# Kernel tuning notes

Hardware: AMD Instinct MI355X
Metric: run time of the kernel (lower is better)

Reference implementation:

```python
import jax, jax.numpy as jnp
import numpy as np

N_USERS, N_ITEMS = 6000, 4000
EPS = 1e-8


def _cosine_similarity(X):
    # rows of X normalized to unit length, then dense gram matrix [n, n]
    norms = jnp.linalg.norm(X, axis=1, keepdims=True) + EPS
    Xn = X / norms
    return Xn @ Xn.T


def _top_k_adjacency(S, k):
    # faithful, vectorized version of the per-row Python loop in the torch code:
    # take top-(k+1), drop the self index, keep the first k remaining entries,
    # scatter values into a sparse-pattern adjacency, then symmetrize.
    n = S.shape[0]
    k_actual = min(k + 1, n)
    vals, idx = jax.lax.top_k(S, k_actual)          # [n, k+1]
    rows = jnp.arange(n)[:, None]                    # [n, 1]
    valid = idx != rows                              # exclude self
    # keep only the first k valid entries per row ( [:k] truncation in torch )
    keep = valid & (jnp.cumsum(valid, axis=1) <= k)
    vals = jnp.where(keep, vals, 0.0)
    adj = jnp.zeros_like(S).at[rows, idx].set(vals)  # indices distinct per row
    return (adj + adj.T) * 0.5


def _sym_normalize(A):
    row_sums = A.sum(axis=1, keepdims=True) + EPS
    col_sums = A.sum(axis=0, keepdims=True) + EPS
    return A / jnp.sqrt(row_sums) / jnp.sqrt(col_sums)


def setup_inputs() -> dict:
    key = jax.random.key(0)
    R = jax.random.uniform(key, (N_USERS, N_ITEMS), dtype=jnp.float32)
    return {"R": R, "k_users": 50, "k_items": 20}


def reference(R, k_users, k_items):
    # user-user graph from cosine similarity over interaction rows
    user_adj = _sym_normalize(_top_k_adjacency(_cosine_similarity(R), k_users))
    # item-item graph from cosine similarity over interaction columns
    item_adj = _sym_normalize(_top_k_adjacency(_cosine_similarity(R.T), k_items))
    # two-sided spectral-style propagation of the interaction signal
    out = user_adj @ (R @ item_adj)                  # [n_users, n_items]
    return out
```

## Files before the change

kernel.cpp:

```cpp
#include <hip/hip_runtime.h>
#include <math.h>

#define EPS 1e-8f

constexpr int N_USERS = 6000;
constexpr int N_ITEMS = 4000;
constexpr int NU_P = 6016;
constexpr int NI_P = 4096;

typedef __bf16 bf16_8 __attribute__((ext_vector_type(8)));
typedef float f32_4 __attribute__((ext_vector_type(4)));
typedef int i32x4 __attribute__((ext_vector_type(4)));

__device__ __forceinline__ void stage16(const void* g, void* l) {
  __builtin_amdgcn_global_load_lds(
      (const __attribute__((address_space(1))) void*)g,
      (__attribute__((address_space(3))) void*)l, 16, 0, 0);
}

__device__ __forceinline__ int xcd_swz(int p, int nwg) {
  return (p & 7) * (nwg >> 3) + (p >> 3);
}

__device__ __forceinline__ void tri_decode(int p, int& by, int& bx) {
  int r = (int)((sqrtf(8.f * p + 1.f) - 1.f) * 0.5f);
  while ((r + 1) * (r + 2) / 2 <= p) r++;
  while (r * (r + 1) / 2 > p) r--;
  by = r;
  bx = p - r * (r + 1) / 2;
}

__device__ __forceinline__ void grp_decode(int p, int nby, int nbx, int& by,
                                           int& bx) {
  const int G = 8;
  const int wide = G * nbx;
  const int band = p / wide;
  const int rem = p - band * wide;
  const int h = min(G, nby - band * G);
  by = band * G + rem % h;
  bx = rem / h;
}

template <int KK, int LDA, int LDB, int LDC, int OUTBF16>
__global__ __launch_bounds__(256) void mfma_prop_bf16(
    const __bf16* __restrict__ A, const __bf16* __restrict__ B,
    float* __restrict__ Cf, __bf16* __restrict__ Cb, int M, int N, int nby,
    int nbx) {
  __shared__ __bf16 sA[2][128 * 32];
  __shared__ __bf16 sB[2][128 * 32];

  int by, bx;
  grp_decode(xcd_swz(blockIdx.x, gridDim.x), nby, nbx, by, bx);

  const int tid = threadIdx.x;
  const int lane = tid & 63;
  const int wave = tid >> 6;
  const int wm = (wave >> 1) * 64;
  const int wn = (wave & 1) * 64;
  const int lm = lane & 15;
  const int kg = lane >> 4;
  const long row0 = (long)by * 128;
  const long col0 = (long)bx * 128;

  f32_4 acc[4][4];
#pragma unroll
  for (int i = 0; i < 4; i++)
#pragma unroll
    for (int j = 0; j < 4; j++) acc[i][j] = (f32_4){0.f, 0.f, 0.f, 0.f};

  const int c0 = tid, c1 = tid + 256;
  const int r0c = c0 >> 2, j0c = ((c0 & 3) - (r0c >> 1)) & 3;
  const int r1c = c1 >> 2, j1c = ((c1 & 3) - (r1c >> 1)) & 3;

  int offA[4], offB[4];
#pragma unroll
  for (int i = 0; i < 4; i++) {
    const int ra = wm + i * 16 + lm;
    const int rb = wn + i * 16 + lm;
    offA[i] = (ra * 4 + ((kg + (ra >> 1)) & 3)) * 8;
    offB[i] = (rb * 4 + ((kg + (rb >> 1)) & 3)) * 8;
  }

  const __bf16* a0 = A + (row0 + r0c) * LDA + j0c * 8;
  const __bf16* a1 = A + (row0 + r1c) * LDA + j1c * 8;
  const __bf16* b0 = B + (col0 + r0c) * LDB + j0c * 8;
  const __bf16* b1 = B + (col0 + r1c) * LDB + j1c * 8;

  for (int k0 = 0; k0 < KK; k0 += 64) {
    stage16(a0 + k0, &sA[0][c0 * 8]);
    stage16(a1 + k0, &sA[0][c1 * 8]);
    stage16(b0 + k0, &sB[0][c0 * 8]);
    stage16(b1 + k0, &sB[0][c1 * 8]);
    stage16(a0 + k0 + 32, &sA[1][c0 * 8]);
    stage16(a1 + k0 + 32, &sA[1][c1 * 8]);
    stage16(b0 + k0 + 32, &sB[1][c0 * 8]);
    stage16(b1 + k0 + 32, &sB[1][c1 * 8]);
    __syncthreads();

#pragma unroll
    for (int h = 0; h < 2; h++) {
      bf16_8 a[4], b[4];
#pragma unroll
      for (int i = 0; i < 4; i++) {
        a[i] = *(const bf16_8*)&sA[h][offA[i]];
        b[i] = *(const bf16_8*)&sB[h][offB[i]];
      }
#pragma unroll
      for (int i = 0; i < 4; i++)
#pragma unroll
        for (int j = 0; j < 4; j++)
          acc[i][j] = __builtin_amdgcn_mfma_f32_16x16x32_bf16(a[i], b[j],
                                                              acc[i][j], 0, 0,
                                                              0);
    }
    __syncthreads();
  }

#pragma unroll
  for (int i = 0; i < 4; i++)
#pragma unroll
    for (int j = 0; j < 4; j++)
#pragma unroll
      for (int r = 0; r < 4; r++) {
        const long gm = row0 + wm + i * 16 + kg * 4 + r;
        const long gn = col0 + wn + j * 16 + lm;
        if (gm < M && gn < N) {
          if (OUTBF16)
            Cb[gm * LDC + gn] = (__bf16)acc[i][j][r];
          else
            Cf[gm * LDC + gn] = acc[i][j][r];
        }
      }
}

template <int KK, int LD, int LDC>
__global__ __launch_bounds__(256) void mfma_gram_i8(
    const signed char* __restrict__ Q, const float* __restrict__ sv,
    float* __restrict__ C, int Nn, float negq) {
  __shared__ signed char sA[2][128 * 64];
  __shared__ signed char sB[2][128 * 64];

  int by, bx;
  tri_decode(xcd_swz(blockIdx.x, gridDim.x), by, bx);

  const int tid = threadIdx.x;
  const int lane = tid & 63;
  const int wave = tid >> 6;
  const int wm = (wave >> 1) * 64;
  const int wn = (wave & 1) * 64;
  const int lm = lane & 15;
  const int kg = lane >> 4;
  const long row0 = (long)by * 128;
  const long col0 = (long)bx * 128;
  const float scale = 1.f / (254.f * 254.f);

  i32x4 acc[4][4];
#pragma unroll
  for (int i = 0; i < 4; i++)
#pragma unroll
    for (int j = 0; j < 4; j++) acc[i][j] = (i32x4){0, 0, 0, 0};

  const int c0 = tid, c1 = tid + 256;
  const int r0c = c0 >> 2, j0c = ((c0 & 3) - (r0c >> 1)) & 3;
  const int r1c = c1 >> 2, j1c = ((c1 & 3) - (r1c >> 1)) & 3;

  int offA[4], offB[4];
#pragma unroll
  for (int i = 0; i < 4; i++) {
    const int ra = wm + i * 16 + lm;
    const int rb = wn + i * 16 + lm;
    offA[i] = (ra * 4 + ((kg + (ra >> 1)) & 3)) * 16;
    offB[i] = (rb * 4 + ((kg + (rb >> 1)) & 3)) * 16;
  }

  const signed char* a0 = Q + (row0 + r0c) * LD + j0c * 16;
  const signed char* a1 = Q + (row0 + r1c) * LD + j1c * 16;
  const signed char* b0 = Q + (col0 + r0c) * LD + j0c * 16;
  const signed char* b1 = Q + (col0 + r1c) * LD + j1c * 16;

  for (int k0 = 0; k0 < KK; k0 += 128) {
    stage16(a0 + k0, &sA[0][c0 * 16]);
    stage16(a1 + k0, &sA[0][c1 * 16]);
    stage16(b0 + k0, &sB[0][c0 * 16]);
    stage16(b1 + k0, &sB[0][c1 * 16]);
    stage16(a0 + k0 + 64, &sA[1][c0 * 16]);
    stage16(a1 + k0 + 64, &sA[1][c1 * 16]);
    stage16(b0 + k0 + 64, &sB[1][c0 * 16]);
    stage16(b1 + k0 + 64, &sB[1][c1 * 16]);
    __syncthreads();

#pragma unroll
    for (int h = 0; h < 2; h++) {
      i32x4 a[4], b[4];
#pragma unroll
      for (int i = 0; i < 4; i++) {
        a[i] = *(const i32x4*)&sA[h][offA[i]];
        b[i] = *(const i32x4*)&sB[h][offB[i]];
      }
#pragma unroll
      for (int i = 0; i < 4; i++)
#pragma unroll
        for (int j = 0; j < 4; j++)
          acc[i][j] = __builtin_amdgcn_mfma_i32_16x16x64_i8(a[i], b[j],
                                                            acc[i][j], 0, 0, 0);
    }
    __syncthreads();
  }

#pragma unroll
  for (int i = 0; i < 4; i++)
#pragma unroll
    for (int j = 0; j < 4; j++)
#pragma unroll
      for (int r = 0; r < 4; r++) {
        const long gm = row0 + wm + i * 16 + kg * 4 + r;
        const long gn = col0 + wn + j * 16 + lm;
        if (gm < Nn && gn < Nn)
          C[gm * LDC + gn] = fmaf((float)acc[i][j][r], scale,
                                  0.5f * (sv[gm] + sv[gn]) + negq);
      }
}

__global__ __launch_bounds__(256) void pad_quant_kernel(
    const float* __restrict__ R, __bf16* __restrict__ H,
    signed char* __restrict__ Qp, int M, int N, int Np) {
  const int r = blockIdx.y;
  const int c = blockIdx.x * 256 + threadIdx.x;
  if (c >= Np) return;
  const bool in = (r < M && c < N);
  const float v = in ? R[(long)r * N + c] : 0.f;
  H[(long)r * Np + c] = (__bf16)v;
  Qp[(long)r * Np + c] =
      in ? (signed char)__float2int_rn((v - 0.5f) * 254.f) : (signed char)0;
}

__global__ __launch_bounds__(256) void transpose_quant_kernel(
    const float* __restrict__ R, signed char* __restrict__ Qp, int M, int N,
    int Mp, int Np) {
  __shared__ float tile[32][33];
  const int tx = threadIdx.x & 31;
  const int ty = threadIdx.x >> 5;
  const int ri = blockIdx.y * 32;
  const int ci = blockIdx.x * 32;
#pragma unroll
  for (int k = 0; k < 4; k++) {
    const int r = ri + ty + k * 8, c = ci + tx;
    tile[ty + k * 8][tx] = (r < M && c < N) ? R[(long)r * N + c] : 0.f;
  }
  __syncthreads();
#pragma unroll
  for (int k = 0; k < 4; k++) {
    const int orow = ci + ty + k * 8;
    const int ocol = ri + tx;
    if (orow < Np && ocol < Mp) {
      const bool in = (orow < N && ocol < M);
      const float v = tile[tx][ty + k * 8];
      Qp[(long)orow * Mp + ocol] =
          in ? (signed char)__float2int_rn((v - 0.5f) * 254.f) : (signed char)0;
    }
  }
}

__global__ __launch_bounds__(256) void mirror_kernel(float* __restrict__ S,
                                                     int n) {
  __shared__ float tile[32][33];
  int by, bx;
  tri_decode(blockIdx.x, by, bx);
  const int tj = by + 1, ti = bx;
  const int sr = tj * 32, sc = ti * 32;
  const int tx = threadIdx.x & 31;
  const int ty = threadIdx.x >> 5;
#pragma unroll
  for (int k = 0; k < 4; k++) {
    const int r = sr + ty + k * 8, c = sc + tx;
    tile[ty + k * 8][tx] = (r < n && c < n) ? S[(long)r * n + c] : 0.f;
  }
  __syncthreads();
#pragma unroll
  for (int k = 0; k < 4; k++) {
    const int r = sc + ty + k * 8, c = sr + tx;
    if (r < n && c < n) S[(long)r * n + c] = tile[tx][ty + k * 8];
  }
}

__global__ __launch_bounds__(256) void row_norm_sum(
    const float* __restrict__ R, float* __restrict__ inv_n,
    float* __restrict__ sv, int M, int K) {
  __shared__ float redA[256];
  __shared__ float redB[256];
  const int row = blockIdx.x;
  float s2 = 0.f, s1 = 0.f;
  for (int j = threadIdx.x; j < K; j += 256) {
    const float v = R[(long)row * K + j];
    s2 = fmaf(v, v, s2);
    s1 += v;
  }
  redA[threadIdx.x] = s2;
  redB[threadIdx.x] = s1;
  __syncthreads();
  for (int o = 128; o > 0; o >>= 1) {
    if (threadIdx.x < o) {
      redA[threadIdx.x] += redA[threadIdx.x + o];
      redB[threadIdx.x] += redB[threadIdx.x + o];
    }
    __syncthreads();
  }
  if (threadIdx.x == 0) {
    inv_n[row] = 1.f / (sqrtf(redA[0]) + EPS);
    sv[row] = redB[0];
  }
}

__global__ __launch_bounds__(256) void col_sums_kernel(
    const float* __restrict__ R, float* __restrict__ acc2,
    float* __restrict__ acc1, int M, int N, int rows_per_chunk) {
  const int j = blockIdx.x * 256 + threadIdx.x;
  if (j >= N) return;
  const int r0 = blockIdx.y * rows_per_chunk;
  const int r1 = min(M, r0 + rows_per_chunk);
  float s2 = 0.f, s1 = 0.f;
  for (int i = r0; i < r1; i++) {
    const float v = R[(long)i * N + j];
    s2 = fmaf(v, v, s2);
    s1 += v;
  }
  atomicAdd(&acc2[j], s2);
  atomicAdd(&acc1[j], s1);
}

__global__ __launch_bounds__(256) void inv_norm_finalize(
    const float* __restrict__ acc, float* __restrict__ inv_n, int n) {
  const int i = blockIdx.x * 256 + threadIdx.x;
  if (i < n) inv_n[i] = 1.f / (sqrtf(acc[i]) + EPS);
}

__global__ __launch_bounds__(64) void topk_kernel(
    float* __restrict__ G, const float* __restrict__ inv_n,
    __bf16* __restrict__ adj, float* __restrict__ rowsum,
    float* __restrict__ colsum, int n, int np, const int* __restrict__ kptr) {
  const int row = blockIdx.x;
  const int lane = threadIdx.x;
  const int k = *kptr;
  const float invr = inv_n[row];

  float v0 = -INFINITY, v1 = -INFINITY, v2 = -INFINITY, v3 = -INFINITY;
  int i0 = n, i1 = n, i2 = n, i3 = n;

  for (int j = lane; j < n; j += 64) {
    const float v =
        (j == row) ? -INFINITY : G[(long)row * n + j] * invr * inv_n[j];
    if (v > v3) {
      if (v > v1) {
        if (v > v0) {
          v3 = v2; i3 = i2; v2 = v1; i2 = i1; v1 = v0; i1 = i0; v0 = v; i0 = j;
        } else {
          v3 = v2; i3 = i2; v2 = v1; i2 = i1; v1 = v; i1 = j;
        }
      } else {
        if (v > v2) {
          v3 = v2; i3 = i2; v2 = v; i2 = j;
        } else {
          v3 = v; i3 = j;
        }
      }
    }
  }

  float rsum = 0.f;
  for (int t = 0; t < k; t++) {
    float v = v0;
    int i = i0;
#pragma unroll
    for (int off = 32; off > 0; off >>= 1) {
      const float ov = __shfl_xor(v, off);
      const int oi = __shfl_xor(i, off);
      if (ov > v || (ov == v && oi < i)) { v = ov; i = oi; }
    }
    if (lane == 0) {
      adj[(long)row * np + i] = (__bf16)v;
      atomicAdd(&colsum[i], v);
      rsum += v;
    }
    if ((i & 63) == lane) {
      G[(long)row * n + i] = -INFINITY;
      v0 = v1; i0 = i1; v1 = v2; i1 = i2; v2 = v3; i2 = i3;
      v3 = -INFINITY; i3 = n;
      if (i0 == n) {
        for (int j = lane; j < n; j += 64) {
          const float vv =
              (j == row) ? -INFINITY : G[(long)row * n + j] * invr * inv_n[j];
          if (vv > v3) {
            if (vv > v1) {
              if (vv > v0) {
                v3 = v2; i3 = i2; v2 = v1; i2 = i1; v1 = v0; i1 = i0;
                v0 = vv; i0 = j;
              } else {
                v3 = v2; i3 = i2; v2 = v1; i2 = i1; v1 = vv; i1 = j;
              }
            } else {
              if (vv > v2) {
                v3 = v2; i3 = i2; v2 = vv; i2 = j;
              } else {
                v3 = vv; i3 = j;
              }
            }
          }
        }
      }
    }
  }
  if (lane == 0) rowsum[row] = rsum;
}

__global__ __launch_bounds__(256) void finalize_kernel(
    const float* __restrict__ rs, const float* __restrict__ cs,
    float* __restrict__ f, int n) {
  const int i = blockIdx.x * 256 + threadIdx.x;
  if (i < n) f[i] = rsqrtf(0.5f * (rs[i] + cs[i]) + EPS);
}

__global__ __launch_bounds__(256) void symscale_kernel(
    __bf16* __restrict__ adj, const float* __restrict__ f, int n, int np) {
  const long idx = (long)blockIdx.x * 256 + threadIdx.x;
  if (idx >= (long)np * np) return;
  const int i = (int)(idx / np);
  const int j = (int)(idx % np);
  if (j <= i || i >= n || j >= n) return;
  const float a = (float)adj[(long)i * np + j];
  const float b = (float)adj[(long)j * np + i];
  const float m = 0.5f * (a + b) * f[i] * f[j];
  adj[(long)i * np + j] = (__bf16)m;
  adj[(long)j * np + i] = (__bf16)m;
}

extern "C" void kernel_launch(void* const* d_in, const int* in_sizes, int n_in,
                              void* d_out, int out_size, void* d_ws,
                              size_t ws_size, hipStream_t stream) {
  const float* R = (const float*)d_in[0];
  const int* k_users_p = (const int*)d_in[1];
  const int* k_items_p = (const int*)d_in[2];
  float* out = (float*)d_out;
  const int NU = N_USERS, NI = N_ITEMS;

  char* ws = (char*)d_ws;
  float* invNu = (float*)(ws + 0);
  float* invNi = (float*)(ws + 32768);
  float* rsU = (float*)(ws + 65536);
  float* csU = (float*)(ws + 98304);
  float* rsI = (float*)(ws + 131072);
  float* csI = (float*)(ws + 163840);
  float* fU = (float*)(ws + 196608);
  float* fI = (float*)(ws + 229376);
  float* nrmI = (float*)(ws + 262144);
  float* svU = (float*)(ws + 294912);
  float* svI = (float*)(ws + 327680);
  const long MB = 1000000L;
  __bf16* Rh = (__bf16*)(ws + 1 * MB);
  signed char* Uh = (signed char*)(ws + 51 * MB);
  float* Su = (float*)(ws + 77 * MB);
  signed char* IhT = (signed char*)(ws + 103 * MB);
  float* Si = (float*)(ws + 128 * MB);
  __bf16* adjIb = (__bf16*)(ws + 222 * MB);
  __bf16* adjUb = (__bf16*)(ws + 256 * MB);
  __bf16* Tt = (__bf16*)(ws + 77 * MB);

  row_norm_sum<<<NU, 256, 0, stream>>>(R, invNu, svU, NU, NI);
  hipMemsetAsync(nrmI, 0, NI * sizeof(float), stream);
  hipMemsetAsync(svI, 0, NI * sizeof(float), stream);
  col_sums_kernel<<<dim3((NI + 255) / 256, 60), 256, 0, stream>>>(R, nrmI, svI,
                                                                  NU, NI, 100);
  inv_norm_finalize<<<(NI + 255) / 256, 256, 0, stream>>>(nrmI, invNi, NI);
  pad_quant_kernel<<<dim3(NI_P / 256, NU_P), 256, 0, stream>>>(R, Rh, Uh, NU,
                                                               NI, NI_P);
  transpose_quant_kernel<<<dim3(NI_P / 32, NU_P / 32), 256, 0, stream>>>(
      R, IhT, NU, NI, NU_P, NI_P);

  mfma_gram_i8<NU_P, NU_P, N_ITEMS><<<32 * 33 / 2, 256, 0, stream>>>(
      IhT, svI, Si, NI, -0.25f * (float)NU);
  {
    const int T = (NI + 31) / 32;
    mirror_kernel<<<T * (T - 1) / 2, 256, 0, stream>>>(Si, NI);
  }
  hipMemsetAsync(adjIb, 0, (long)NI_P * NI_P * sizeof(__bf16), stream);
  hipMemsetAsync(csI, 0, NI * sizeof(float), stream);
  topk_kernel<<<NI, 64, 0, stream>>>(Si, invNi, adjIb, rsI, csI, NI, NI_P,
                                     k_items_p);
  finalize_kernel<<<(NI + 255) / 256, 256, 0, stream>>>(rsI, csI, fI, NI);
  {
    const long tot = (long)NI_P * NI_P;
    symscale_kernel<<<(tot + 255) / 256, 256, 0, stream>>>(adjIb, fI, NI, NI_P);
  }

  mfma_gram_i8<NI_P, NI_P, N_USERS><<<47 * 48 / 2, 256, 0, stream>>>(
      Uh, svU, Su, NU, -0.25f * (float)NI);
  {
    const int T = (NU + 31) / 32;
    mirror_kernel<<<T * (T - 1) / 2, 256, 0, stream>>>(Su, NU);
  }
  hipMemsetAsync(adjUb, 0, (long)NU_P * NU_P * sizeof(__bf16), stream);
  hipMemsetAsync(csU, 0, NU * sizeof(float), stream);
  topk_kernel<<<NU, 64, 0, stream>>>(Su, invNu, adjUb, rsU, csU, NU, NU_P,
                                     k_users_p);
  finalize_kernel<<<(NU + 255) / 256, 256, 0, stream>>>(rsU, csU, fU, NU);
  {
    const long tot = (long)NU_P * NU_P;
    symscale_kernel<<<(tot + 255) / 256, 256, 0, stream>>>(adjUb, fU, NU, NU_P);
  }

  mfma_prop_bf16<NI_P, NI_P, NI_P, NU_P, 1><<<32 * 47, 256, 0, stream>>>(
      adjIb, Rh, nullptr, Tt, NI_P, NU_P, 32, 47);
  mfma_prop_bf16<NU_P, NU_P, NU_P, N_ITEMS, 0><<<47 * 32, 256, 0, stream>>>(
      adjUb, Tt, out, nullptr, NU, NI, 47, 32);
}
```

Measured before the change: 1.780 ms.

## Double-buffer LDS staging to overlap global loads with MFMA compute

Both GEMM kernels change from loading two K-halves and then computing them behind a barrier to a ping-pong pipeline. The next K-slice is staged asynchronously into the alternate LDS buffer while the current slice is computed, with one barrier per step. The goal is to hide global-to-LDS latency behind MFMA work. In exchange there are twice as many loop iterations and barriers per unit of K, and each iteration stages less data.

```diff
diff --git a/kernel.cpp b/kernel.cpp
--- a/kernel.cpp
+++ b/kernel.cpp
@@ -86,35 +86,37 @@
   const __bf16* b0 = B + (col0 + r0c) * LDB + j0c * 8;
   const __bf16* b1 = B + (col0 + r1c) * LDB + j1c * 8;
 
-  for (int k0 = 0; k0 < KK; k0 += 64) {
-    stage16(a0 + k0, &sA[0][c0 * 8]);
-    stage16(a1 + k0, &sA[0][c1 * 8]);
-    stage16(b0 + k0, &sB[0][c0 * 8]);
-    stage16(b1 + k0, &sB[0][c1 * 8]);
-    stage16(a0 + k0 + 32, &sA[1][c0 * 8]);
-    stage16(a1 + k0 + 32, &sA[1][c1 * 8]);
-    stage16(b0 + k0 + 32, &sB[1][c0 * 8]);
-    stage16(b1 + k0 + 32, &sB[1][c1 * 8]);
+  auto stage_phase = [&](int buf, int k0) {
+    stage16(a0 + k0, &sA[buf][c0 * 8]);
+    stage16(a1 + k0, &sA[buf][c1 * 8]);
+    stage16(b0 + k0, &sB[buf][c0 * 8]);
+    stage16(b1 + k0, &sB[buf][c1 * 8]);
+  };
+  auto compute_phase = [&](int buf) {
+    bf16_8 a[4], b[4];
+#pragma unroll
+    for (int i = 0; i < 4; i++) {
+      a[i] = *(const bf16_8*)&sA[buf][offA[i]];
+      b[i] = *(const bf16_8*)&sB[buf][offB[i]];
+    }
+#pragma unroll
+    for (int i = 0; i < 4; i++)
+#pragma unroll
+      for (int j = 0; j < 4; j++)
+        acc[i][j] = __builtin_amdgcn_mfma_f32_16x16x32_bf16(a[i], b[j],
+                                                            acc[i][j], 0, 0, 0);
+  };
+
+  stage_phase(0, 0);
+  __syncthreads();
+  int cur = 0;
+  for (int k0 = 32; k0 < KK; k0 += 32) {
+    stage_phase(cur ^ 1, k0);
+    compute_phase(cur);
     __syncthreads();
-
-#pragma unroll
-    for (int h = 0; h < 2; h++) {
-      bf16_8 a[4], b[4];
-#pragma unroll
-      for (int i = 0; i < 4; i++) {
-        a[i] = *(const bf16_8*)&sA[h][offA[i]];
-        b[i] = *(const bf16_8*)&sB[h][offB[i]];
-      }
-#pragma unroll
-      for (int i = 0; i < 4; i++)
-#pragma unroll
-        for (int j = 0; j < 4; j++)
-          acc[i][j] = __builtin_amdgcn_mfma_f32_16x16x32_bf16(a[i], b[j],
-                                                              acc[i][j], 0, 0,
-                                                              0);
-    }
-    __syncthreads();
-  }
+    cur ^= 1;
+  }
+  compute_phase(cur);
 
 #pragma unroll
   for (int i = 0; i < 4; i++)
@@ -178,34 +180,37 @@
   const signed char* b0 = Q + (col0 + r0c) * LD + j0c * 16;
   const signed char* b1 = Q + (col0 + r1c) * LD + j1c * 16;
 
-  for (int k0 = 0; k0 < KK; k0 += 128) {
-    stage16(a0 + k0, &sA[0][c0 * 16]);
-    stage16(a1 + k0, &sA[0][c1 * 16]);
-    stage16(b0 + k0, &sB[0][c0 * 16]);
-    stage16(b1 + k0, &sB[0][c1 * 16]);
-    stage16(a0 + k0 + 64, &sA[1][c0 * 16]);
-    stage16(a1 + k0 + 64, &sA[1][c1 * 16]);
-    stage16(b0 + k0 + 64, &sB[1][c0 * 16]);
-    stage16(b1 + k0 + 64, &sB[1][c1 * 16]);
+  auto stage_phase = [&](int buf, int k0) {
+    stage16(a0 + k0, &sA[buf][c0 * 16]);
+    stage16(a1 + k0, &sA[buf][c1 * 16]);
+    stage16(b0 + k0, &sB[buf][c0 * 16]);
+    stage16(b1 + k0, &sB[buf][c1 * 16]);
+  };
+  auto compute_phase = [&](int buf) {
+    i32x4 a[4], b[4];
+#pragma unroll
+    for (int i = 0; i < 4; i++) {
+      a[i] = *(const i32x4*)&sA[buf][offA[i]];
+      b[i] = *(const i32x4*)&sB[buf][offB[i]];
+    }
+#pragma unroll
+    for (int i = 0; i < 4; i++)
+#pragma unroll
+      for (int j = 0; j < 4; j++)
+        acc[i][j] = __builtin_amdgcn_mfma_i32_16x16x64_i8(a[i], b[j],
+                                                          acc[i][j], 0, 0, 0);
+  };
+
+  stage_phase(0, 0);
+  __syncthreads();
+  int cur = 0;
+  for (int k0 = 64; k0 < KK; k0 += 64) {
+    stage_phase(cur ^ 1, k0);
+    compute_phase(cur);
     __syncthreads();
-
-#pragma unroll
-    for (int h = 0; h < 2; h++) {
-      i32x4 a[4], b[4];
-#pragma unroll
-      for (int i = 0; i < 4; i++) {
-        a[i] = *(const i32x4*)&sA[h][offA[i]];
-        b[i] = *(const i32x4*)&sB[h][offB[i]];
-      }
-#pragma unroll
-      for (int i = 0; i < 4; i++)
-#pragma unroll
-        for (int j = 0; j < 4; j++)
-          acc[i][j] = __builtin_amdgcn_mfma_i32_16x16x64_i8(a[i], b[j],
-                                                            acc[i][j], 0, 0, 0);
-    }
-    __syncthreads();
-  }
+    cur ^= 1;
+  }
+  compute_phase(cur);
 
 #pragma unroll
   for (int i = 0; i < 4; i++)
```

Result: no change. 1.787 ms (+0.4%).

## Double-buffer LDS staging in bf16 and int8 GEMM mainloops

Applied to the files above, without the earlier changes.

Both GEMM kernels used to load two K-halves into LDS, wait at a barrier, then compute, so global-to-LDS loads never overlapped the MFMA work. The loops are now software-pipelined with two LDS buffers: the next chunk is staged into one buffer while the other is consumed, with a prologue and epilogue. This aims to hide global load latency behind matrix math. The risk is a race: the compute on the current buffer is not separated by a barrier from the async global_load_lds writes into the other buffer, and the fill issued just before each compute runs with no vmcnt wait before the following barrier.

```diff
diff --git a/kernel.cpp b/kernel.cpp
--- a/kernel.cpp
+++ b/kernel.cpp
@@ -86,35 +86,44 @@
   const __bf16* b0 = B + (col0 + r0c) * LDB + j0c * 8;
   const __bf16* b1 = B + (col0 + r1c) * LDB + j1c * 8;
 
-  for (int k0 = 0; k0 < KK; k0 += 64) {
-    stage16(a0 + k0, &sA[0][c0 * 8]);
-    stage16(a1 + k0, &sA[0][c1 * 8]);
-    stage16(b0 + k0, &sB[0][c0 * 8]);
-    stage16(b1 + k0, &sB[0][c1 * 8]);
-    stage16(a0 + k0 + 32, &sA[1][c0 * 8]);
-    stage16(a1 + k0 + 32, &sA[1][c1 * 8]);
-    stage16(b0 + k0 + 32, &sB[1][c0 * 8]);
-    stage16(b1 + k0 + 32, &sB[1][c1 * 8]);
+#define PROP_STAGE(BUF, K0)                  \
+  do {                                       \
+    stage16(a0 + (K0), &sA[BUF][c0 * 8]);    \
+    stage16(a1 + (K0), &sA[BUF][c1 * 8]);    \
+    stage16(b0 + (K0), &sB[BUF][c0 * 8]);    \
+    stage16(b1 + (K0), &sB[BUF][c1 * 8]);    \
+  } while (0)
+
+#define PROP_COMPUTE(BUF)                                                   \
+  do {                                                                      \
+    bf16_8 a[4], b[4];                                                      \
+    _Pragma("unroll") for (int i = 0; i < 4; i++) {                         \
+      a[i] = *(const bf16_8*)&sA[BUF][offA[i]];                             \
+      b[i] = *(const bf16_8*)&sB[BUF][offB[i]];                             \
+    }                                                                       \
+    _Pragma("unroll") for (int i = 0; i < 4; i++) _Pragma("unroll") for (   \
+        int j = 0; j < 4; j++) acc[i][j] =                                  \
+        __builtin_amdgcn_mfma_f32_16x16x32_bf16(a[i], b[j], acc[i][j], 0,   \
+                                                0, 0);                      \
+  } while (0)
+
+  PROP_STAGE(0, 0);
+  __syncthreads();
+  for (int k0 = 32; k0 < KK - 32; k0 += 64) {
+    PROP_STAGE(1, k0);
+    PROP_COMPUTE(0);
     __syncthreads();
-
-#pragma unroll
-    for (int h = 0; h < 2; h++) {
-      bf16_8 a[4], b[4];
-#pragma unroll
-      for (int i = 0; i < 4; i++) {
-        a[i] = *(const bf16_8*)&sA[h][offA[i]];
-        b[i] = *(const bf16_8*)&sB[h][offB[i]];
-      }
-#pragma unroll
-      for (int i = 0; i < 4; i++)
-#pragma unroll
-        for (int j = 0; j < 4; j++)
-          acc[i][j] = __builtin_amdgcn_mfma_f32_16x16x32_bf16(a[i], b[j],
-                                                              acc[i][j], 0, 0,
-                                                              0);
-    }
+    PROP_STAGE(0, k0 + 32);
+    PROP_COMPUTE(1);
     __syncthreads();
   }
+  PROP_STAGE(1, KK - 32);
+  PROP_COMPUTE(0);
+  __syncthreads();
+  PROP_COMPUTE(1);
+
+#undef PROP_STAGE
+#undef PROP_COMPUTE
 
 #pragma unroll
   for (int i = 0; i < 4; i++)
@@ -178,34 +187,44 @@
   const signed char* b0 = Q + (col0 + r0c) * LD + j0c * 16;
   const signed char* b1 = Q + (col0 + r1c) * LD + j1c * 16;
 
-  for (int k0 = 0; k0 < KK; k0 += 128) {
-    stage16(a0 + k0, &sA[0][c0 * 16]);
-    stage16(a1 + k0, &sA[0][c1 * 16]);
-    stage16(b0 + k0, &sB[0][c0 * 16]);
-    stage16(b1 + k0, &sB[0][c1 * 16]);
-    stage16(a0 + k0 + 64, &sA[1][c0 * 16]);
-    stage16(a1 + k0 + 64, &sA[1][c1 * 16]);
-    stage16(b0 + k0 + 64, &sB[1][c0 * 16]);
-    stage16(b1 + k0 + 64, &sB[1][c1 * 16]);
+#define GRAM_STAGE(BUF, K0)                   \
+  do {                                        \
+    stage16(a0 + (K0), &sA[BUF][c0 * 16]);    \
+    stage16(a1 + (K0), &sA[BUF][c1 * 16]);    \
+    stage16(b0 + (K0), &sB[BUF][c0 * 16]);    \
+    stage16(b1 + (K0), &sB[BUF][c1 * 16]);    \
+  } while (0)
+
+#define GRAM_COMPUTE(BUF)                                                 \
+  do {                                                                    \
+    i32x4 a[4], b[4];                                                     \
+    _Pragma("unroll") for (int i = 0; i < 4; i++) {                       \
+      a[i] = *(const i32x4*)&sA[BUF][offA[i]];                            \
+      b[i] = *(const i32x4*)&sB[BUF][offB[i]];                            \
+    }                                                                     \
+    _Pragma("unroll") for (int i = 0; i < 4; i++) _Pragma("unroll") for ( \
+        int j = 0; j < 4; j++) acc[i][j] =                                \
+        __builtin_amdgcn_mfma_i32_16x16x64_i8(a[i], b[j], acc[i][j], 0,   \
+                                              0, 0);                      \
+  } while (0)
+
+  GRAM_STAGE(0, 0);
+  __syncthreads();
+  for (int k0 = 64; k0 < KK - 64; k0 += 128) {
+    GRAM_STAGE(1, k0);
+    GRAM_COMPUTE(0);
     __syncthreads();
-
-#pragma unroll
-    for (int h = 0; h < 2; h++) {
-      i32x4 a[4], b[4];
-#pragma unroll
-      for (int i = 0; i < 4; i++) {
-        a[i] = *(const i32x4*)&sA[h][offA[i]];
-        b[i] = *(const i32x4*)&sB[h][offB[i]];
-      }
-#pragma unroll
-      for (int i = 0; i < 4; i++)
-#pragma unroll
-        for (int j = 0; j < 4; j++)
-          acc[i][j] = __builtin_amdgcn_mfma_i32_16x16x64_i8(a[i], b[j],
-                                                            acc[i][j], 0, 0, 0);
-    }
+    GRAM_STAGE(0, k0 + 64);
+    GRAM_COMPUTE(1);
     __syncthreads();
   }
+  GRAM_STAGE(1, KK - 64);
+  GRAM_COMPUTE(0);
+  __syncthreads();
+  GRAM_COMPUTE(1);
+
+#undef GRAM_STAGE
+#undef GRAM_COMPUTE
 
 #pragma unroll
   for (int i = 0; i < 4; i++)
```

New measurement: 2.020 ms. 13.5% more time.
